# Performance work log

Hardware: AMD Instinct MI355X
Metric: run time of the kernel (lower is better)

The kernel has to match this reference:

```python
import jax, jax.numpy as jnp
import numpy as np


def setup_inputs() -> dict:
    key = jax.random.key(0)
    k1, k2, k3 = jax.random.split(key, 3)
    B, H, F, O = 2048, 512, 128, 10
    inputs = jax.random.normal(k1, (B, F), dtype=jnp.float32)
    # centers ~ uniform(-1, 1) as in init_params
    centers = jax.random.uniform(k2, (H, F), dtype=jnp.float32, minval=-1.0, maxval=1.0)
    sigma = jnp.ones((1,), dtype=jnp.float32)
    W = jax.random.normal(k3, (O, H), dtype=jnp.float32) * (1.0 / np.sqrt(H))
    b = jnp.zeros((O,), dtype=jnp.float32)
    return {"inputs": inputs, "centers": centers, "sigma": sigma, "W": W, "b": b}


def reference(inputs, centers, sigma, W, b):
    # pairwise squared distances: [B, H, F] diff -> sum over F -> [B, H]
    diff = inputs[:, None, :] - centers[None, :, :]
    distances = jnp.sum(diff * diff, axis=-1)  # [B, H]
    rbf = jnp.exp(-distances / (2.0 * sigma[0] ** 2))  # [B, H]
    # linear: y = rbf @ W.T + b
    return rbf @ W.T + b
```

## Files before the change

### kernel.cpp

```cpp
#include <hip/hip_runtime.h>


constexpr int Fdim = 128;
constexpr int Hdim = 512;
constexpr int Odim = 10;
constexpr int BM   = 8;
constexpr int KC   = 32;
constexpr int NCH  = Fdim / KC;
constexpr int LDC  = 513;
constexpr int LDXT = 12;
constexpr int LDR  = 516;

__global__ __launch_bounds__(512, 1) void rbf_all(
    const float* __restrict__ x,
    const float* __restrict__ c,
    const float* __restrict__ sigmap,
    const float* __restrict__ W,
    const float* __restrict__ bias,
    float* __restrict__ out)
{
    __shared__ float cT[KC][LDC];
    __shared__ float xT[Fdim][LDXT];
    __shared__ float rbf_s[BM][LDR];
    __shared__ float po_s[BM][8][Odim];
    __shared__ float xn_s[BM];
    __shared__ float cn_s[Hdim];

    const int tid  = threadIdx.x;
    const int lane = tid & 63;
    const int wave = tid >> 6;
    const int wr   = wave >> 2;
    const int wh   = wave & 3;
    const int row0 = blockIdx.x * BM;

    const float4* x4 = reinterpret_cast<const float4*>(x);
    const float4* c4 = reinterpret_cast<const float4*>(c);

    if (tid < 256) {
        int r  = tid >> 5;
        int fq = tid & 31;
        float4 v = x4[(size_t)(row0 + r) * (Fdim / 4) + fq];
        xT[4 * fq + 0][r] = v.x;
        xT[4 * fq + 1][r] = v.y;
        xT[4 * fq + 2][r] = v.z;
        xT[4 * fq + 3][r] = v.w;
        float s = v.x * v.x + v.y * v.y + v.z * v.z + v.w * v.w;
#pragma unroll
        for (int sft = 1; sft < 32; sft <<= 1) s += __shfl_xor(s, sft, 64);
        if (fq == 0) xn_s[r] = s;
    }

    const int f4 = tid & 7;
    const int hh = tid >> 3;

    float4 pre[8];
    float cn_part[8];
#pragma unroll
    for (int p = 0; p < 8; ++p) cn_part[p] = 0.0f;

#pragma unroll
    for (int p = 0; p < 8; ++p)
        pre[p] = c4[(size_t)(hh + 64 * p) * (Fdim / 4) + f4];
#pragma unroll
    for (int p = 0; p < 8; ++p) {
        float4 v = pre[p];
        int h = hh + 64 * p;
        cT[4 * f4 + 0][h] = v.x;
        cT[4 * f4 + 1][h] = v.y;
        cT[4 * f4 + 2][h] = v.z;
        cT[4 * f4 + 3][h] = v.w;
        cn_part[p] += v.x * v.x + v.y * v.y + v.z * v.z + v.w * v.w;
    }
    __syncthreads();

    float acc[4][2];
#pragma unroll
    for (int i = 0; i < 4; ++i) { acc[i][0] = 0.0f; acc[i][1] = 0.0f; }

    for (int k = 0; k < NCH; ++k) {
        if (k + 1 < NCH) {
#pragma unroll
            for (int p = 0; p < 8; ++p)
                pre[p] = c4[(size_t)(hh + 64 * p) * (Fdim / 4) + (k + 1) * (KC / 4) + f4];
        }

#pragma unroll 8
        for (int f = 0; f < KC; ++f) {
            float4 xv = *reinterpret_cast<const float4*>(&xT[k * KC + f][4 * wr]);
            float2 cv = *reinterpret_cast<const float2*>(&cT[f][wh * 128 + 2 * lane]);
            acc[0][0] = fmaf(xv.x, cv.x, acc[0][0]);
            acc[0][1] = fmaf(xv.x, cv.y, acc[0][1]);
            acc[1][0] = fmaf(xv.y, cv.x, acc[1][0]);
            acc[1][1] = fmaf(xv.y, cv.y, acc[1][1]);
            acc[2][0] = fmaf(xv.z, cv.x, acc[2][0]);
            acc[2][1] = fmaf(xv.z, cv.y, acc[2][1]);
            acc[3][0] = fmaf(xv.w, cv.x, acc[3][0]);
            acc[3][1] = fmaf(xv.w, cv.y, acc[3][1]);
        }

        if (k + 1 < NCH) {
            __syncthreads();
#pragma unroll
            for (int p = 0; p < 8; ++p) {
                float4 v = pre[p];
                int h = hh + 64 * p;
                cT[4 * f4 + 0][h] = v.x;
                cT[4 * f4 + 1][h] = v.y;
                cT[4 * f4 + 2][h] = v.z;
                cT[4 * f4 + 3][h] = v.w;
                cn_part[p] += v.x * v.x + v.y * v.y + v.z * v.z + v.w * v.w;
            }
            __syncthreads();
        }
    }

    float2 W2[Odim][4];
#pragma unroll
    for (int o = 0; o < Odim; ++o)
#pragma unroll
        for (int kk = 0; kk < 4; ++kk)
            W2[o][kk] = *reinterpret_cast<const float2*>(
                &W[o * Hdim + 2 * lane + 128 * kk]);

#pragma unroll
    for (int p = 0; p < 8; ++p) {
        float s = cn_part[p];
        s += __shfl_xor(s, 1, 64);
        s += __shfl_xor(s, 2, 64);
        s += __shfl_xor(s, 4, 64);
        cn_part[p] = s;
    }
    if (f4 == 0) {
#pragma unroll
        for (int p = 0; p < 8; ++p) cn_s[hh + 64 * p] = cn_part[p];
    }
    __syncthreads();

    const float sg    = sigmap[0];
    const float scale = -1.0f / (2.0f * sg * sg);
    {
        float2 cn = *reinterpret_cast<const float2*>(&cn_s[wh * 128 + 2 * lane]);
#pragma unroll
        for (int i = 0; i < 4; ++i) {
            float xn = xn_s[4 * wr + i];
            float2 rv;
            rv.x = __expf((xn + cn.x - 2.0f * acc[i][0]) * scale);
            rv.y = __expf((xn + cn.y - 2.0f * acc[i][1]) * scale);
            *reinterpret_cast<float2*>(&rbf_s[4 * wr + i][wh * 128 + 2 * lane]) = rv;
        }
    }
    __syncthreads();

    {
        const int row = wave;
        float po[Odim];
#pragma unroll
        for (int o = 0; o < Odim; ++o) po[o] = 0.0f;

#pragma unroll
        for (int kk = 0; kk < 4; ++kk) {
            float2 rv = *reinterpret_cast<const float2*>(
                &rbf_s[row][2 * lane + 128 * kk]);
#pragma unroll
            for (int o = 0; o < Odim; ++o) {
                po[o] = fmaf(rv.x, W2[o][kk].x, po[o]);
                po[o] = fmaf(rv.y, W2[o][kk].y, po[o]);
            }
        }
#pragma unroll
        for (int s = 1; s < 8; s <<= 1) {
#pragma unroll
            for (int o = 0; o < Odim; ++o)
                po[o] += __shfl_xor(po[o], s, 64);
        }
        if ((lane & 7) == 0) {
#pragma unroll
            for (int o = 0; o < Odim; ++o)
                po_s[row][lane >> 3][o] = po[o];
        }
    }
    __syncthreads();

    if (tid < BM * Odim) {
        int w = tid / Odim;
        int o = tid - w * Odim;
        float v = bias[o];
#pragma unroll
        for (int g = 0; g < 8; ++g) v += po_s[w][g][o];
        out[(size_t)(row0 + w) * Odim + o] = v;
    }
}

extern "C" void kernel_launch(void* const* d_in, const int* in_sizes, int n_in,
                              void* d_out, int out_size, void* d_ws, size_t ws_size,
                              hipStream_t stream) {
    const float* x  = (const float*)d_in[0];
    const float* c  = (const float*)d_in[1];
    const float* sg = (const float*)d_in[2];
    const float* W  = (const float*)d_in[3];
    const float* b  = (const float*)d_in[4];
    float* out      = (float*)d_out;

    const int B = in_sizes[0] / Fdim;

    rbf_all<<<B / BM, 512, 0, stream>>>(x, c, sg, W, b, out);
}
```

Measured before the change: 17.88 us.

## Split feature dimension across wave halves with shared-memory partial-sum reduction

Waves now split each 32-wide feature chunk into two halves instead of splitting the 8 rows, so every wave computes all 8 rows for its half of the features. The x read becomes a broadcast of 8 values per feature step, and the number of c loads per FMA is halved. Partial sums from the second half are stored to rbf_s and added by the first-half waves before the exp. This adds a shared-memory reduction and doubles accumulator registers, and only half the waves run the exp stage.

```diff
diff --git a/kernel.cpp b/kernel.cpp
--- a/kernel.cpp
+++ b/kernel.cpp
@@ -29,7 +29,7 @@
     const int tid  = threadIdx.x;
     const int lane = tid & 63;
     const int wave = tid >> 6;
-    const int wr   = wave >> 2;
+    const int fh   = wave >> 2;
     const int wh   = wave & 3;
     const int row0 = blockIdx.x * BM;
 
@@ -73,9 +73,9 @@
     }
     __syncthreads();
 
-    float acc[4][2];
-#pragma unroll
-    for (int i = 0; i < 4; ++i) { acc[i][0] = 0.0f; acc[i][1] = 0.0f; }
+    float acc[8][2];
+#pragma unroll
+    for (int r = 0; r < 8; ++r) { acc[r][0] = 0.0f; acc[r][1] = 0.0f; }
 
     for (int k = 0; k < NCH; ++k) {
         if (k + 1 < NCH) {
@@ -84,18 +84,29 @@
                 pre[p] = c4[(size_t)(hh + 64 * p) * (Fdim / 4) + (k + 1) * (KC / 4) + f4];
         }
 
-#pragma unroll 8
-        for (int f = 0; f < KC; ++f) {
-            float4 xv = *reinterpret_cast<const float4*>(&xT[k * KC + f][4 * wr]);
-            float2 cv = *reinterpret_cast<const float2*>(&cT[f][wh * 128 + 2 * lane]);
-            acc[0][0] = fmaf(xv.x, cv.x, acc[0][0]);
-            acc[0][1] = fmaf(xv.x, cv.y, acc[0][1]);
-            acc[1][0] = fmaf(xv.y, cv.x, acc[1][0]);
-            acc[1][1] = fmaf(xv.y, cv.y, acc[1][1]);
-            acc[2][0] = fmaf(xv.z, cv.x, acc[2][0]);
-            acc[2][1] = fmaf(xv.z, cv.y, acc[2][1]);
-            acc[3][0] = fmaf(xv.w, cv.x, acc[3][0]);
-            acc[3][1] = fmaf(xv.w, cv.y, acc[3][1]);
+#pragma unroll
+        for (int f16 = 0; f16 < KC / 2; ++f16) {
+            const int fl = fh * (KC / 2) + f16;
+            const float* xrow = &xT[k * KC + fl][0];
+            float4 xa = *reinterpret_cast<const float4*>(xrow);
+            float4 xb = *reinterpret_cast<const float4*>(xrow + 4);
+            float2 cv = *reinterpret_cast<const float2*>(&cT[fl][wh * 128 + 2 * lane]);
+            acc[0][0] = fmaf(xa.x, cv.x, acc[0][0]);
+            acc[0][1] = fmaf(xa.x, cv.y, acc[0][1]);
+            acc[1][0] = fmaf(xa.y, cv.x, acc[1][0]);
+            acc[1][1] = fmaf(xa.y, cv.y, acc[1][1]);
+            acc[2][0] = fmaf(xa.z, cv.x, acc[2][0]);
+            acc[2][1] = fmaf(xa.z, cv.y, acc[2][1]);
+            acc[3][0] = fmaf(xa.w, cv.x, acc[3][0]);
+            acc[3][1] = fmaf(xa.w, cv.y, acc[3][1]);
+            acc[4][0] = fmaf(xb.x, cv.x, acc[4][0]);
+            acc[4][1] = fmaf(xb.x, cv.y, acc[4][1]);
+            acc[5][0] = fmaf(xb.y, cv.x, acc[5][0]);
+            acc[5][1] = fmaf(xb.y, cv.y, acc[5][1]);
+            acc[6][0] = fmaf(xb.z, cv.x, acc[6][0]);
+            acc[6][1] = fmaf(xb.z, cv.y, acc[6][1]);
+            acc[7][0] = fmaf(xb.w, cv.x, acc[7][0]);
+            acc[7][1] = fmaf(xb.w, cv.y, acc[7][1]);
         }
 
         if (k + 1 < NCH) {
@@ -122,6 +133,14 @@
             W2[o][kk] = *reinterpret_cast<const float2*>(
                 &W[o * Hdim + 2 * lane + 128 * kk]);
 
+    if (fh == 1) {
+#pragma unroll
+        for (int r = 0; r < 8; ++r) {
+            float2 m; m.x = acc[r][0]; m.y = acc[r][1];
+            *reinterpret_cast<float2*>(&rbf_s[r][wh * 128 + 2 * lane]) = m;
+        }
+    }
+
 #pragma unroll
     for (int p = 0; p < 8; ++p) {
         float s = cn_part[p];
@@ -138,15 +157,18 @@
 
     const float sg    = sigmap[0];
     const float scale = -1.0f / (2.0f * sg * sg);
-    {
+    if (fh == 0) {
         float2 cn = *reinterpret_cast<const float2*>(&cn_s[wh * 128 + 2 * lane]);
 #pragma unroll
-        for (int i = 0; i < 4; ++i) {
-            float xn = xn_s[4 * wr + i];
+        for (int r = 0; r < 8; ++r) {
+            float2 m = *reinterpret_cast<const float2*>(&rbf_s[r][wh * 128 + 2 * lane]);
+            float xn = xn_s[r];
+            float d0 = xn + cn.x - 2.0f * (acc[r][0] + m.x);
+            float d1 = xn + cn.y - 2.0f * (acc[r][1] + m.y);
             float2 rv;
-            rv.x = __expf((xn + cn.x - 2.0f * acc[i][0]) * scale);
-            rv.y = __expf((xn + cn.y - 2.0f * acc[i][1]) * scale);
-            *reinterpret_cast<float2*>(&rbf_s[4 * wr + i][wh * 128 + 2 * lane]) = rv;
+            rv.x = __expf(d0 * scale);
+            rv.y = __expf(d1 * scale);
+            *reinterpret_cast<float2*>(&rbf_s[r][wh * 128 + 2 * lane]) = rv;
         }
     }
     __syncthreads();
```

After: 18.98 us. 6.1% more time.
